# Kernel optimization log

Hardware: AMD Instinct MI355X
Metric: run time of the kernel (lower is better)

The kernel has to match this reference:

```python
import jax, jax.numpy as jnp
import numpy as np

B, H, W, C = 2, 64, 64, 192
NUM_HEADS = 6
K = 7  # kernel_size, dilation = 1


def setup_inputs() -> dict:
    key = jax.random.key(0)
    ks = jax.random.split(key, 5)
    return {
        "x": jax.random.normal(ks[0], (B, H, W, C), dtype=jnp.float32),
        "w_qkv": jax.random.normal(ks[1], (3 * C, C), dtype=jnp.float32) * 0.02,
        "rpb": jax.random.normal(ks[2], (NUM_HEADS, 2 * K - 1, 2 * K - 1), dtype=jnp.float32) * 0.02,
        "temperature": jnp.ones((NUM_HEADS,), dtype=jnp.float32),
        "w_proj": jax.random.normal(ks[3], (C, C), dtype=jnp.float32) * 0.02,
    }


def reference(x, w_qkv, rpb, temperature, w_proj):
    b, h, w, c = x.shape
    hd = c // NUM_HEADS
    scale = hd ** (-0.5)

    # 1x1 conv qkv projection (pointwise linear over channels)
    qkv = jnp.einsum("bhwc,dc->bhwd", x, w_qkv)
    qkv = qkv.reshape(b, h, w, 3, NUM_HEADS, hd).transpose(3, 0, 4, 1, 2, 5)
    q, k, v = qkv[0], qkv[1], qkv[2]  # (B, nH, H, W, hd)
    q = q * scale

    # NATTEN neighborhood: window centered at each pixel, clamped to stay in-bounds
    si = jnp.clip(jnp.arange(h) - K // 2, 0, h - K)
    rows = si[:, None] + jnp.arange(K)          # (H, K) neighbor row indices
    sj = jnp.clip(jnp.arange(w) - K // 2, 0, w - K)
    cols = sj[:, None] + jnp.arange(K)          # (W, K) neighbor col indices

    # gather key/value neighborhoods: (B, nH, H, K, W, K, hd)
    k_nb = k[:, :, rows][:, :, :, :, cols]
    v_nb = v[:, :, rows][:, :, :, :, cols]

    # QK: (B, nH, H, W, Kh, Kw)
    attn = jnp.einsum("bnijd,bnikjld->bnijkl", q, k_nb)

    # relative position bias: index = neighbor - query + (K-1)
    ri = rows - jnp.arange(h)[:, None] + (K - 1)  # (H, K)
    rj = cols - jnp.arange(w)[:, None] + (K - 1)  # (W, K)
    bias = rpb[:, ri][:, :, :, rj]                # (nH, H, K, W, K)
    bias = bias.transpose(0, 1, 3, 2, 4)          # (nH, H, W, K, K)
    attn = attn + bias[None]

    attn = attn.reshape(b, NUM_HEADS, h, w, K * K)
    attn = attn * temperature[None, :, None, None, None]
    attn = jax.nn.softmax(attn, axis=-1)

    v_nb = v_nb.transpose(0, 1, 2, 4, 3, 5, 6).reshape(b, NUM_HEADS, h, w, K * K, hd)
    out = jnp.einsum("bnijp,bnijpd->bnijd", attn, v_nb)
    out = out.transpose(0, 2, 3, 1, 4).reshape(b, h, w, c)

    # 1x1 conv output projection
    return jnp.einsum("bhwc,dc->bhwd", out, w_proj)
```

## Files before the change

kernel.cpp:

```cpp
#include <hip/hip_runtime.h>
#include <hip/hip_bf16.h>
#include <math.h>

#define BB 2
#define HH 64
#define WW 64
#define CC 192
#define NH 6
#define HD 32
#define KS 7
#define NPIX (BB * HH * WW)
#define SCALE 0.17677669529663687f
#define GK 192

typedef __attribute__((ext_vector_type(8))) _Float16 f16x8;
typedef __attribute__((ext_vector_type(4))) float    f32x4;

#define LDA 200

__global__ __launch_bounds__(256) void gemm_mfma(const float* __restrict__ A,
                                                 const float* __restrict__ Bw,
                                                 float* __restrict__ Cm,
                                                 int M, int N) {
    __shared__ _Float16 As[64 * LDA];
    __shared__ _Float16 Bs[64 * LDA];

    const int t    = threadIdx.x;
    const int row0 = blockIdx.x * 64;
    const int col0 = blockIdx.y * 64;

#pragma unroll
    for (int it = 0; it < 6; ++it) {
        const int idx = t + it * 256;
        const int r   = idx / 24;
        const int c8  = (idx % 24) * 8;
        const float* pa = A  + (size_t)(row0 + r) * GK + c8;
        const float* pb = Bw + (size_t)(col0 + r) * GK + c8;
        float4 a0 = *(const float4*)pa;
        float4 a1 = *(const float4*)(pa + 4);
        float4 b0 = *(const float4*)pb;
        float4 b1 = *(const float4*)(pb + 4);
        f16x8 ha, hb;
        ha[0] = (_Float16)a0.x; ha[1] = (_Float16)a0.y;
        ha[2] = (_Float16)a0.z; ha[3] = (_Float16)a0.w;
        ha[4] = (_Float16)a1.x; ha[5] = (_Float16)a1.y;
        ha[6] = (_Float16)a1.z; ha[7] = (_Float16)a1.w;
        hb[0] = (_Float16)b0.x; hb[1] = (_Float16)b0.y;
        hb[2] = (_Float16)b0.z; hb[3] = (_Float16)b0.w;
        hb[4] = (_Float16)b1.x; hb[5] = (_Float16)b1.y;
        hb[6] = (_Float16)b1.z; hb[7] = (_Float16)b1.w;
        *(f16x8*)&As[r * LDA + c8] = ha;
        *(f16x8*)&Bs[r * LDA + c8] = hb;
    }
    __syncthreads();

    const int wave = t >> 6;
    const int wr   = wave >> 1;
    const int wc   = wave & 1;
    const int lane = t & 63;
    const int ln   = lane & 15;
    const int quad = lane >> 4;

    f32x4 acc[2][2] = {};

#pragma unroll
    for (int ks = 0; ks < 6; ++ks) {
        const int k0 = ks * 32 + quad * 8;
        f16x8 af[2], bf[2];
#pragma unroll
        for (int mi = 0; mi < 2; ++mi)
            af[mi] = *(const f16x8*)&As[(wr * 32 + mi * 16 + ln) * LDA + k0];
#pragma unroll
        for (int ni = 0; ni < 2; ++ni)
            bf[ni] = *(const f16x8*)&Bs[(wc * 32 + ni * 16 + ln) * LDA + k0];
#pragma unroll
        for (int mi = 0; mi < 2; ++mi)
#pragma unroll
            for (int ni = 0; ni < 2; ++ni)
                acc[mi][ni] = __builtin_amdgcn_mfma_f32_16x16x32_f16(
                    af[mi], bf[ni], acc[mi][ni], 0, 0, 0);
    }

#pragma unroll
    for (int mi = 0; mi < 2; ++mi)
#pragma unroll
        for (int ni = 0; ni < 2; ++ni) {
            const int col = col0 + wc * 32 + ni * 16 + ln;
#pragma unroll
            for (int r = 0; r < 4; ++r) {
                const int row = row0 + wr * 32 + mi * 16 + quad * 4 + r;
                Cm[(size_t)row * N + col] = acc[mi][ni][r];
            }
        }
}

#define STRK 33
#define STRV 17
#define VOFF 2112
#define REGDW 3200
#define PSTR 34

__device__ __forceinline__ unsigned bf16r(float x) {
    unsigned u = __float_as_uint(x);
    return (u + 0x7fffu + ((u >> 16) & 1u)) >> 16;
}

__global__ __launch_bounds__(256, 3) void natten_v2(const float* __restrict__ qkv,
                                                    const float* __restrict__ rpb,
                                                    const float* __restrict__ temperature,
                                                    float* __restrict__ out) {
    const int tid  = threadIdx.x;
    const int w    = tid >> 6;
    const int j    = tid & 63;
    const int i    = blockIdx.x & 63;
    const int head = (blockIdx.x >> 6) % NH;
    const int b    = blockIdx.x / (64 * NH);

    __shared__ float region[4][REGDW];
    __shared__ float srpb[169];
    if (tid < 169) srpb[tid] = rpb[head * 169 + tid];

    const float temp = temperature[head];
    const size_t pix = (size_t)b * 4096 + i * 64 + j;
    const float* qp = qkv + pix * 576 + head * HD;

    float q[HD];
#pragma unroll
    for (int d4 = 0; d4 < 8; ++d4) {
        float4 f = *(const float4*)(qp + d4 * 4);
        q[d4 * 4 + 0] = f.x * SCALE; q[d4 * 4 + 1] = f.y * SCALE;
        q[d4 * 4 + 2] = f.z * SCALE; q[d4 * 4 + 3] = f.w * SCALE;
    }

    __syncthreads();

    const int si = min(max(i - 3, 0), HH - KS);
    const int sj = min(max(j - 3, 0), WW - KS);

    float m = -1e30f, l = 0.f;
    float acc[HD];
#pragma unroll
    for (int d = 0; d < HD; ++d) acc[d] = 0.f;

    float*    kreg = region[w];
    unsigned* vreg = (unsigned*)(region[w] + VOFF);

    const int nrows = (w < 3) ? 2 : 1;
    for (int t = 0; t < nrows; ++t) {
        const int ki = 2 * w + t;
        const int ni = si + ki;

        const float* rowk = qkv + ((size_t)b * 4096 + (size_t)ni * 64) * 576 + CC + head * HD;
#pragma unroll
        for (int it = 0; it < 8; ++it) {
            const int idx = j + (it << 6);
            const int px = idx >> 3, d4 = idx & 7;
            const float* src = rowk + px * 576 + d4 * 4;
            float4 kf = *(const float4*)src;
            float4 vf = *(const float4*)(src + CC);
            float* kd = kreg + px * STRK + d4 * 4;
            kd[0] = kf.x; kd[1] = kf.y; kd[2] = kf.z; kd[3] = kf.w;
            unsigned* vd = vreg + px * STRV + d4 * 2;
            vd[0] = bf16r(vf.x) | (bf16r(vf.y) << 16);
            vd[1] = bf16r(vf.z) | (bf16r(vf.w) << 16);
        }

        const float* rb = srpb + (ni - i + 6) * 13;
#pragma unroll
        for (int kj = 0; kj < 7; ++kj) {
            const int nj = sj + kj;
            const float* kk = kreg + nj * STRK;
            float dot = 0.f;
#pragma unroll
            for (int d = 0; d < HD; ++d) dot = fmaf(q[d], kk[d], dot);
            const float logit = (dot + rb[nj - j + 6]) * temp;

            const float mn    = fmaxf(m, logit);
            const float alpha = __expf(m - mn);
            const float p     = __expf(logit - mn);
            l = l * alpha + p;
            m = mn;

            const unsigned* vv = vreg + nj * STRV;
#pragma unroll
            for (int c = 0; c < 16; ++c) {
                const unsigned u = vv[c];
                const float lo = __uint_as_float(u << 16);
                const float hi = __uint_as_float(u & 0xffff0000u);
                acc[2 * c + 0] = fmaf(acc[2 * c + 0], alpha, p * lo);
                acc[2 * c + 1] = fmaf(acc[2 * c + 1], alpha, p * hi);
            }
        }
    }

    if (w > 0) {
        float* pp = region[w] + j * PSTR;
#pragma unroll
        for (int d = 0; d < HD; ++d) pp[d] = acc[d];
        pp[32] = m; pp[33] = l;
    }
    __syncthreads();
    if (w == 0) {
#pragma unroll
        for (int ww = 1; ww < 4; ++ww) {
            const float* pp = region[ww] + j * PSTR;
            const float m2 = pp[32], l2 = pp[33];
            const float mn = fmaxf(m, m2);
            const float a1 = __expf(m - mn), a2 = __expf(m2 - mn);
            l = l * a1 + l2 * a2;
#pragma unroll
            for (int d = 0; d < HD; ++d) acc[d] = acc[d] * a1 + pp[d] * a2;
            m = mn;
        }
        const float inv = 1.f / l;
        float* op = out + pix * CC + head * HD;
#pragma unroll
        for (int d4 = 0; d4 < 8; ++d4) {
            float4 o = make_float4(acc[d4 * 4 + 0] * inv, acc[d4 * 4 + 1] * inv,
                                   acc[d4 * 4 + 2] * inv, acc[d4 * 4 + 3] * inv);
            *(float4*)(op + d4 * 4) = o;
        }
    }
}

extern "C" void kernel_launch(void* const* d_in, const int* in_sizes, int n_in,
                              void* d_out, int out_size, void* d_ws, size_t ws_size,
                              hipStream_t stream) {
    const float* x           = (const float*)d_in[0];
    const float* w_qkv       = (const float*)d_in[1];
    const float* rpb         = (const float*)d_in[2];
    const float* temperature = (const float*)d_in[3];
    const float* w_proj      = (const float*)d_in[4];
    float* out = (float*)d_out;

    float* qkv      = (float*)d_ws;
    float* attn_out = qkv + (size_t)NPIX * 3 * CC;

    gemm_mfma<<<dim3(NPIX / 64, (3 * CC) / 64), 256, 0, stream>>>(
        x, w_qkv, qkv, NPIX, 3 * CC);

    natten_v2<<<dim3(BB * NH * HH), 256, 0, stream>>>(
        qkv, rpb, temperature, attn_out);

    gemm_mfma<<<dim3(NPIX / 64, CC / 64), 256, 0, stream>>>(
        attn_out, w_proj, out, NPIX, CC);
}
```

Baseline: 111.2 us.

## Store QKV and attention intermediates in fp16 and use packed dot products

```diff
diff --git a/kernel.cpp b/kernel.cpp
--- a/kernel.cpp
+++ b/kernel.cpp
@@ -1,5 +1,4 @@
 #include <hip/hip_runtime.h>
-#include <hip/hip_bf16.h>
 #include <math.h>
 
 #define BB 2
@@ -14,20 +13,37 @@
 #define GK 192
 
 typedef __attribute__((ext_vector_type(8))) _Float16 f16x8;
+typedef __attribute__((ext_vector_type(2))) _Float16 f16x2;
 typedef __attribute__((ext_vector_type(4))) float    f32x4;
 
 #define LDA 200
-
-__global__ __launch_bounds__(256) void gemm_mfma(const float* __restrict__ A,
-                                                 const float* __restrict__ Bw,
-                                                 float* __restrict__ Cm,
-                                                 int M, int N) {
-    __shared__ _Float16 As[64 * LDA];
-    __shared__ _Float16 Bs[64 * LDA];
-
-    const int t    = threadIdx.x;
-    const int row0 = blockIdx.x * 64;
-    const int col0 = blockIdx.y * 64;
+#define CST 68
+
+__device__ __forceinline__ f16x2 u2h(unsigned u) {
+    union { unsigned u; f16x2 h; } c; c.u = u; return c.h;
+}
+
+__device__ __forceinline__ float hdot2(f16x2 a, f16x2 b, float c) {
+#if __has_builtin(__builtin_amdgcn_fdot2)
+    return __builtin_amdgcn_fdot2(a, b, c, false);
+#else
+    return fmaf((float)a[1], (float)b[1], fmaf((float)a[0], (float)b[0], c));
+#endif
+}
+
+__global__ __launch_bounds__(256) void gemm_qkv(const float* __restrict__ A,
+                                                const float* __restrict__ Bw,
+                                                _Float16* __restrict__ Cm) {
+    __shared__ __align__(16) _Float16 As[64 * LDA];
+    __shared__ __align__(16) _Float16 Bs[64 * LDA];
+
+    const int t  = threadIdx.x;
+    const int s  = blockIdx.x;
+    const int kk = s >> 3;
+    const int rowblk = (s & 7) * 16 + kk / 9;
+    const int colblk = kk % 9;
+    const int row0 = rowblk * 64;
+    const int col0 = colblk * 64;
 
 #pragma unroll
     for (int it = 0; it < 6; ++it) {
@@ -81,55 +97,75 @@
                     af[mi], bf[ni], acc[mi][ni], 0, 0, 0);
     }
 
+    __syncthreads();
+    float* Cs = (float*)As;
 #pragma unroll
     for (int mi = 0; mi < 2; ++mi)
 #pragma unroll
         for (int ni = 0; ni < 2; ++ni) {
-            const int col = col0 + wc * 32 + ni * 16 + ln;
+            const int col = wc * 32 + ni * 16 + ln;
 #pragma unroll
             for (int r = 0; r < 4; ++r) {
-                const int row = row0 + wr * 32 + mi * 16 + quad * 4 + r;
-                Cm[(size_t)row * N + col] = acc[mi][ni][r];
+                const int row = wr * 32 + mi * 16 + quad * 4 + r;
+                Cs[row * CST + col] = acc[mi][ni][r];
             }
         }
-}
-
-#define STRK 33
-#define STRV 17
-#define VOFF 2112
-#define REGDW 3200
-#define PSTR 34
-
-__device__ __forceinline__ unsigned bf16r(float x) {
-    unsigned u = __float_as_uint(x);
-    return (u + 0x7fffu + ((u >> 16) & 1u)) >> 16;
-}
-
-__global__ __launch_bounds__(256, 3) void natten_v2(const float* __restrict__ qkv,
+    __syncthreads();
+
+    const float sc = (col0 < 192) ? SCALE : 1.f;
+#pragma unroll
+    for (int it = 0; it < 2; ++it) {
+        const int idx = t + it * 256;
+        const int r   = idx >> 3;
+        const int c8  = (idx & 7) * 8;
+        const float* src = Cs + r * CST + c8;
+        float4 f0 = *(const float4*)src;
+        float4 f1 = *(const float4*)(src + 4);
+        f16x8 hv;
+        hv[0] = (_Float16)(f0.x * sc); hv[1] = (_Float16)(f0.y * sc);
+        hv[2] = (_Float16)(f0.z * sc); hv[3] = (_Float16)(f0.w * sc);
+        hv[4] = (_Float16)(f1.x * sc); hv[5] = (_Float16)(f1.y * sc);
+        hv[6] = (_Float16)(f1.z * sc); hv[7] = (_Float16)(f1.w * sc);
+        *(f16x8*)&Cm[(size_t)(row0 + r) * 576 + col0 + c8] = hv;
+    }
+}
+
+#define KSTR 66
+#define VOFFD 1056
+#define PSTRF 34
+
+__global__ __launch_bounds__(256, 3) void natten_v3(const _Float16* __restrict__ qkv,
                                                     const float* __restrict__ rpb,
                                                     const float* __restrict__ temperature,
-                                                    float* __restrict__ out) {
+                                                    _Float16* __restrict__ attn) {
     const int tid  = threadIdx.x;
     const int w    = tid >> 6;
     const int j    = tid & 63;
-    const int i    = blockIdx.x & 63;
-    const int head = (blockIdx.x >> 6) % NH;
-    const int b    = blockIdx.x / (64 * NH);
-
-    __shared__ float region[4][REGDW];
+    const int s    = blockIdx.x;
+    const int g    = (s & 7) * 96 + (s >> 3);
+    const int i    = g & 63;
+    const int head = (g >> 6) % NH;
+    const int b    = g / (64 * NH);
+
+    __shared__ unsigned region[4][2176];
     __shared__ float srpb[169];
     if (tid < 169) srpb[tid] = rpb[head * 169 + tid];
 
     const float temp = temperature[head];
     const size_t pix = (size_t)b * 4096 + i * 64 + j;
-    const float* qp = qkv + pix * 576 + head * HD;
-
-    float q[HD];
-#pragma unroll
-    for (int d4 = 0; d4 < 8; ++d4) {
-        float4 f = *(const float4*)(qp + d4 * 4);
-        q[d4 * 4 + 0] = f.x * SCALE; q[d4 * 4 + 1] = f.y * SCALE;
-        q[d4 * 4 + 2] = f.z * SCALE; q[d4 * 4 + 3] = f.w * SCALE;
+    const _Float16* qp = qkv + pix * 576 + head * HD;
+
+    f16x2 q2[16];
+#pragma unroll
+    for (int c8 = 0; c8 < 4; ++c8) {
+        f16x8 qv = *(const f16x8*)(qp + c8 * 8);
+#pragma unroll
+        for (int p2 = 0; p2 < 4; ++p2) {
+            f16x2 tmp;
+            tmp[0] = qv[p2 * 2 + 0];
+            tmp[1] = qv[p2 * 2 + 1];
+            q2[c8 * 4 + p2] = tmp;
+        }
     }
 
     __syncthreads();
@@ -142,37 +178,48 @@
 #pragma unroll
     for (int d = 0; d < HD; ++d) acc[d] = 0.f;
 
-    float*    kreg = region[w];
-    unsigned* vreg = (unsigned*)(region[w] + VOFF);
+    unsigned* kreg = region[w];
+    unsigned* vreg = region[w] + VOFFD;
 
     const int nrows = (w < 3) ? 2 : 1;
     for (int t = 0; t < nrows; ++t) {
         const int ki = 2 * w + t;
         const int ni = si + ki;
 
-        const float* rowk = qkv + ((size_t)b * 4096 + (size_t)ni * 64) * 576 + CC + head * HD;
-#pragma unroll
-        for (int it = 0; it < 8; ++it) {
+        const _Float16* rowk =
+            qkv + ((size_t)b * 4096 + (size_t)ni * 64) * 576 + CC + head * HD;
+#pragma unroll
+        for (int it = 0; it < 4; ++it) {
             const int idx = j + (it << 6);
-            const int px = idx >> 3, d4 = idx & 7;
-            const float* src = rowk + px * 576 + d4 * 4;
-            float4 kf = *(const float4*)src;
-            float4 vf = *(const float4*)(src + CC);
-            float* kd = kreg + px * STRK + d4 * 4;
-            kd[0] = kf.x; kd[1] = kf.y; kd[2] = kf.z; kd[3] = kf.w;
-            unsigned* vd = vreg + px * STRV + d4 * 2;
-            vd[0] = bf16r(vf.x) | (bf16r(vf.y) << 16);
-            vd[1] = bf16r(vf.z) | (bf16r(vf.w) << 16);
+            const int px  = idx >> 2;
+            const int d8  = idx & 3;
+            const _Float16* src = rowk + px * 576 + d8 * 8;
+            f16x8 kf = *(const f16x8*)src;
+            f16x8 vf = *(const f16x8*)(src + CC);
+            uint4 ku = *(const uint4*)&kf;
+            uint4 vu = *(const uint4*)&vf;
+            unsigned* kd = kreg + (d8 * 4) * KSTR + px;
+            kd[0]        = ku.x; kd[KSTR]     = ku.y;
+            kd[2 * KSTR] = ku.z; kd[3 * KSTR] = ku.w;
+            unsigned* vd = vreg + (d8 * 4) * KSTR + px;
+            vd[0]        = vu.x; vd[KSTR]     = vu.y;
+            vd[2 * KSTR] = vu.z; vd[3 * KSTR] = vu.w;
         }
 
         const float* rb = srpb + (ni - i + 6) * 13;
 #pragma unroll
         for (int kj = 0; kj < 7; ++kj) {
             const int nj = sj + kj;
-            const float* kk = kreg + nj * STRK;
-            float dot = 0.f;
-#pragma unroll
-            for (int d = 0; d < HD; ++d) dot = fmaf(q[d], kk[d], dot);
+            const unsigned* kcol = kreg + nj;
+            float d0 = 0.f, d1 = 0.f, d2 = 0.f, d3 = 0.f;
+#pragma unroll
+            for (int c = 0; c < 4; ++c) {
+                d0 = hdot2(q2[c],      u2h(kcol[c * KSTR]),        d0);
+                d1 = hdot2(q2[c + 4],  u2h(kcol[(c + 4) * KSTR]),  d1);
+                d2 = hdot2(q2[c + 8],  u2h(kcol[(c + 8) * KSTR]),  d2);
+                d3 = hdot2(q2[c + 12], u2h(kcol[(c + 12) * KSTR]), d3);
+            }
+            const float dot   = (d0 + d1) + (d2 + d3);
             const float logit = (dot + rb[nj - j + 6]) * temp;
 
             const float mn    = fmaxf(m, logit);
@@ -181,20 +228,18 @@
             l = l * alpha + p;
             m = mn;
 
-            const unsigned* vv = vreg + nj * STRV;
+            const unsigned* vcol = vreg + nj;
 #pragma unroll
             for (int c = 0; c < 16; ++c) {
-                const unsigned u = vv[c];
-                const float lo = __uint_as_float(u << 16);
-                const float hi = __uint_as_float(u & 0xffff0000u);
-                acc[2 * c + 0] = fmaf(acc[2 * c + 0], alpha, p * lo);
-                acc[2 * c + 1] = fmaf(acc[2 * c + 1], alpha, p * hi);
+                const f16x2 h = u2h(vcol[c * KSTR]);
+                acc[2 * c + 0] = fmaf(acc[2 * c + 0], alpha, p * (float)h[0]);
+                acc[2 * c + 1] = fmaf(acc[2 * c + 1], alpha, p * (float)h[1]);
             }
         }
     }
 
     if (w > 0) {
-        float* pp = region[w] + j * PSTR;
+        float* pp = (float*)(region[w]) + j * PSTRF;
 #pragma unroll
         for (int d = 0; d < HD; ++d) pp[d] = acc[d];
         pp[32] = m; pp[33] = l;
@@ -203,7 +248,7 @@
     if (w == 0) {
 #pragma unroll
         for (int ww = 1; ww < 4; ++ww) {
-            const float* pp = region[ww] + j * PSTR;
+            const float* pp = (const float*)(region[ww]) + j * PSTRF;
             const float m2 = pp[32], l2 = pp[33];
             const float mn = fmaxf(m, m2);
             const float a1 = __expf(m - mn), a2 = __expf(m2 - mn);
@@ -213,14 +258,89 @@
             m = mn;
         }
         const float inv = 1.f / l;
-        float* op = out + pix * CC + head * HD;
-#pragma unroll
-        for (int d4 = 0; d4 < 8; ++d4) {
-            float4 o = make_float4(acc[d4 * 4 + 0] * inv, acc[d4 * 4 + 1] * inv,
-                                   acc[d4 * 4 + 2] * inv, acc[d4 * 4 + 3] * inv);
-            *(float4*)(op + d4 * 4) = o;
-        }
-    }
+        _Float16* op = attn + pix * CC + head * HD;
+#pragma unroll
+        for (int c8 = 0; c8 < 4; ++c8) {
+            f16x8 o;
+#pragma unroll
+            for (int e = 0; e < 8; ++e)
+                o[e] = (_Float16)(acc[c8 * 8 + e] * inv);
+            *(f16x8*)(op + c8 * 8) = o;
+        }
+    }
+}
+
+__global__ __launch_bounds__(256) void gemm_proj(const _Float16* __restrict__ A,
+                                                 const float* __restrict__ Bw,
+                                                 float* __restrict__ Cm) {
+    __shared__ __align__(16) _Float16 As[64 * LDA];
+    __shared__ __align__(16) _Float16 Bs[64 * LDA];
+
+    const int t  = threadIdx.x;
+    const int s  = blockIdx.x;
+    const int kk = s >> 3;
+    const int rowblk = (s & 7) * 16 + kk / 3;
+    const int colblk = kk % 3;
+    const int row0 = rowblk * 64;
+    const int col0 = colblk * 64;
+
+#pragma unroll
+    for (int it = 0; it < 6; ++it) {
+        const int idx = t + it * 256;
+        const int r   = idx / 24;
+        const int c8  = (idx % 24) * 8;
+        f16x8 ha = *(const f16x8*)(A + (size_t)(row0 + r) * GK + c8);
+        const float* pb = Bw + (size_t)(col0 + r) * GK + c8;
+        float4 b0 = *(const float4*)pb;
+        float4 b1 = *(const float4*)(pb + 4);
+        f16x8 hb;
+        hb[0] = (_Float16)b0.x; hb[1] = (_Float16)b0.y;
+        hb[2] = (_Float16)b0.z; hb[3] = (_Float16)b0.w;
+        hb[4] = (_Float16)b1.x; hb[5] = (_Float16)b1.y;
+        hb[6] = (_Float16)b1.z; hb[7] = (_Float16)b1.w;
+        *(f16x8*)&As[r * LDA + c8] = ha;
+        *(f16x8*)&Bs[r * LDA + c8] = hb;
+    }
+    __syncthreads();
+
+    const int wave = t >> 6;
+    const int wr   = wave >> 1;
+    const int wc   = wave & 1;
+    const int lane = t & 63;
+    const int ln   = lane & 15;
+    const int quad = lane >> 4;
+
+    f32x4 acc[2][2] = {};
+
+#pragma unroll
+    for (int ks = 0; ks < 6; ++ks) {
+        const int k0 = ks * 32 + quad * 8;
+        f16x8 af[2], bf[2];
+#pragma unroll
+        for (int mi = 0; mi < 2; ++mi)
+            af[mi] = *(const f16x8*)&As[(wr * 32 + mi * 16 + ln) * LDA + k0];
+#pragma unroll
+        for (int ni = 0; ni < 2; ++ni)
+            bf[ni] = *(const f16x8*)&Bs[(wc * 32 + ni * 16 + ln) * LDA + k0];
+#pragma unroll
+        for (int mi = 0; mi < 2; ++mi)
+#pragma unroll
+            for (int ni = 0; ni < 2; ++ni)
+                acc[mi][ni] = __builtin_amdgcn_mfma_f32_16x16x32_f16(
+                    af[mi], bf[ni], acc[mi][ni], 0, 0, 0);
+    }
+
+#pragma unroll
+    for (int mi = 0; mi < 2; ++mi)
+#pragma unroll
+        for (int ni = 0; ni < 2; ++ni) {
+            const int col = col0 + wc * 32 + ni * 16 + ln;
+#pragma unroll
+            for (int r = 0; r < 4; ++r) {
+                const int row = row0 + wr * 32 + mi * 16 + quad * 4 + r;
+                Cm[(size_t)row * CC + col] = acc[mi][ni][r];
+            }
+        }
 }
 
 extern "C" void kernel_launch(void* const* d_in, const int* in_sizes, int n_in,
@@ -233,15 +353,12 @@
     const float* w_proj      = (const float*)d_in[4];
     float* out = (float*)d_out;
 
-    float* qkv      = (float*)d_ws;
-    float* attn_out = qkv + (size_t)NPIX * 3 * CC;
-
-    gemm_mfma<<<dim3(NPIX / 64, (3 * CC) / 64), 256, 0, stream>>>(
-        x, w_qkv, qkv, NPIX, 3 * CC);
-
-    natten_v2<<<dim3(BB * NH * HH), 256, 0, stream>>>(
-        qkv, rpb, temperature, attn_out);
-
-    gemm_mfma<<<dim3(NPIX / 64, CC / 64), 256, 0, stream>>>(
-        attn_out, w_proj, out, NPIX, CC);
-}
+    _Float16* qkv  = (_Float16*)d_ws;
+    _Float16* attn = qkv + (size_t)NPIX * 3 * CC;
+
+    gemm_qkv<<<dim3(1152), 256, 0, stream>>>(x, w_qkv, qkv);
+
+    natten_v3<<<dim3(768), 256, 0, stream>>>(qkv, rpb, temperature, attn);
+
+    gemm_proj<<<dim3(384), 256, 0, stream>>>(attn, w_proj, out);
+}
```

Result: faster. 99.96 us (-10.1%).
